# Kernel optimization log

Measured on AMD Instinct MI355X. Metric: run time of the kernel, lower is better.

The kernel has to match this reference:

```python
import jax, jax.numpy as jnp
import numpy as np

HORIZON = 60
HID = 128

def setup_inputs() -> dict:
    key = jax.random.key(0)
    ks = jax.random.split(key, 7)
    B, D, O = 16384, 256, 3
    s_ih = 1.0 / np.sqrt(HID)
    return {
        "x": jax.random.normal(ks[0], (B, D), jnp.float32),
        "W_ih": jax.random.normal(ks[1], (3 * HID, D), jnp.float32) * s_ih,
        "W_hh": jax.random.normal(ks[2], (3 * HID, HID), jnp.float32) * s_ih,
        "b_ih": jax.random.normal(ks[3], (3 * HID,), jnp.float32) * s_ih,
        "b_hh": jax.random.normal(ks[4], (3 * HID,), jnp.float32) * s_ih,
        "W_out": jax.random.normal(ks[5], (O, HID), jnp.float32) * s_ih,
        "b_out": jax.random.normal(ks[6], (O,), jnp.float32) * s_ih,
    }

def reference(x, W_ih, W_hh, b_ih, b_hh, W_out, b_out):
    # Input is identical at every timestep -> precompute input projection once.
    B = x.shape[0]
    gi = x @ W_ih.T + b_ih                      # [B, 3H]
    gi_r, gi_z, gi_n = jnp.split(gi, 3, axis=-1)

    def step(h, _):
        gh = h @ W_hh.T + b_hh                  # [B, 3H]
        gh_r, gh_z, gh_n = jnp.split(gh, 3, axis=-1)
        r = jax.nn.sigmoid(gi_r + gh_r)
        z = jax.nn.sigmoid(gi_z + gh_z)
        n = jnp.tanh(gi_n + r * gh_n)
        h_new = (1.0 - z) * n + z * h           # torch GRU update
        return h_new, h_new

    h0 = jnp.zeros((B, HID), x.dtype)
    _, hs = jax.lax.scan(step, h0, None, length=HORIZON)   # [T, B, H]
    out = jnp.einsum('tbh,oh->bto', hs, W_out) + b_out     # [B, T, O]
    return out
```

## Files before the change

### kernel.cpp

```cpp
#include <hip/hip_runtime.h>


typedef __attribute__((ext_vector_type(8))) short short8;
typedef __attribute__((ext_vector_type(4))) float f32x4;

#define MFMA16(a, b, c) __builtin_amdgcn_mfma_f32_16x16x32_bf16((a), (b), (c), 0, 0, 0)

__device__ __forceinline__ short f2bf(float x) {
    union { float f; unsigned u; } v; v.f = x;
    unsigned r = v.u + 0x7FFFu + ((v.u >> 16) & 1u);
    return (short)(r >> 16);
}
__device__ __forceinline__ unsigned pk2bf(float lo, float hi) {
    return ((unsigned)(unsigned short)f2bf(hi) << 16) | (unsigned short)f2bf(lo);
}

__device__ __forceinline__ short8 cvt8(const float* __restrict__ p) {
    f32x4 a = *(const f32x4*)p;
    f32x4 b = *(const f32x4*)(p + 4);
    short8 r;
    r[0] = f2bf(a[0]); r[1] = f2bf(a[1]); r[2] = f2bf(a[2]); r[3] = f2bf(a[3]);
    r[4] = f2bf(b[0]); r[5] = f2bf(b[1]); r[6] = f2bf(b[2]); r[7] = f2bf(b[3]);
    return r;
}

__device__ __forceinline__ float fsig(float x) {
    float e = __builtin_amdgcn_exp2f(x * -1.442695041f);
    return __builtin_amdgcn_rcpf(1.0f + e);
}
__device__ __forceinline__ float ftanh_(float x) {
    float e = __builtin_amdgcn_exp2f(x * -2.885390082f);
    return 2.0f * __builtin_amdgcn_rcpf(1.0f + e) - 1.0f;
}

__global__ __launch_bounds__(512, 2) void gru_traj_kernel(
    const float* __restrict__ x,
    const float* __restrict__ W_ih,
    const float* __restrict__ W_hh,
    const float* __restrict__ b_ih,
    const float* __restrict__ b_hh,
    const float* __restrict__ W_out,
    const float* __restrict__ b_out,
    float* __restrict__ out)
{
    const int tid  = threadIdx.x;
    const int wid  = tid >> 6;
    const int lane = tid & 63;
    const int l15  = lane & 15;
    const int l4   = lane >> 4;
    const int b0   = blockIdx.x << 6;
    const int hb   = wid << 4;

    __shared__ short hbuf[2][64 * 128];
    __shared__ short wobuf[3 * 136];

    {
        int* z = (int*)hbuf[0];
        #pragma unroll
        for (int i = 0; i < 8; ++i) z[tid + i * 512] = 0;
    }
    if (tid < 384) wobuf[(tid >> 7) * 136 + (tid & 127)] = f2bf(W_out[tid]);

    short8 wfrag[3][4];
    #pragma unroll
    for (int g = 0; g < 3; ++g)
        #pragma unroll
        for (int kt = 0; kt < 4; ++kt)
            wfrag[g][kt] = cvt8(W_hh + (size_t)(g * 128 + hb + l15) * 128 + kt * 32 + l4 * 8);

    const f32x4 bR4  = *(const f32x4*)(b_ih +       hb + l4 * 4) + *(const f32x4*)(b_hh +       hb + l4 * 4);
    const f32x4 bZ4  = *(const f32x4*)(b_ih + 128 + hb + l4 * 4) + *(const f32x4*)(b_hh + 128 + hb + l4 * 4);
    const f32x4 bN4i = *(const f32x4*)(b_ih + 256 + hb + l4 * 4);
    const f32x4 bN4h = *(const f32x4*)(b_hh + 256 + hb + l4 * 4);
    const float bo0 = b_out[0], bo1 = b_out[1], bo2 = b_out[2];

    f32x4 initR[4], initZ[4], giN[4];
    #pragma unroll
    for (int q = 0; q < 4; ++q) { initR[q] = bR4; initZ[q] = bZ4; giN[q] = bN4i; }
    #pragma unroll
    for (int kt = 0; kt < 8; ++kt) {
        short8 a0 = cvt8(W_ih + (size_t)(      hb + l15) * 256 + kt * 32 + l4 * 8);
        short8 a1 = cvt8(W_ih + (size_t)(128 + hb + l15) * 256 + kt * 32 + l4 * 8);
        short8 a2 = cvt8(W_ih + (size_t)(256 + hb + l15) * 256 + kt * 32 + l4 * 8);
        #pragma unroll
        for (int q = 0; q < 4; ++q) {
            short8 bx = cvt8(x + (size_t)(b0 + q * 16 + l15) * 256 + kt * 32 + l4 * 8);
            initR[q] = MFMA16(a0, bx, initR[q]);
            initZ[q] = MFMA16(a1, bx, initZ[q]);
            giN [q] = MFMA16(a2, bx, giN [q]);
        }
    }

    float hq[4][4];
    #pragma unroll
    for (int q = 0; q < 4; ++q)
        #pragma unroll
        for (int r = 0; r < 4; ++r) hq[q][r] = 0.f;

    const int s8  = (wid << 2) | l4;
    const int wsw = (((s8 >> 1) ^ l15) & 15);

    __syncthreads();

    #pragma unroll 2
    for (int t = 0; t < 60; ++t) {
        const short* rb = hbuf[t & 1];
        short*       wb = hbuf[(t & 1) ^ 1];
        #pragma unroll
        for (int q = 0; q < 4; ++q) {
            short8 af[4];
            #pragma unroll
            for (int kt = 0; kt < 4; ++kt)
                af[kt] = *(const short8*)(rb + (q * 16 + l15) * 128 + (((kt * 4 + l4) ^ l15) & 15) * 8);

            if (t > 0 && wid == ((q + t) & 7)) {
                f32x4 oa = (f32x4){0.f, 0.f, 0.f, 0.f};
                #pragma unroll
                for (int kt = 0; kt < 4; ++kt) {
                    short8 wo = {0, 0, 0, 0, 0, 0, 0, 0};
                    if (l15 < 3) wo = *(const short8*)(wobuf + l15 * 136 + kt * 32 + l4 * 8);
                    oa = MFMA16(wo, af[kt], oa);
                }
                if (l4 == 0) {
                    float* op = out + (size_t)(b0 + q * 16 + l15) * 180 + (t - 1) * 3;
                    op[0] = oa[0] + bo0; op[1] = oa[1] + bo1; op[2] = oa[2] + bo2;
                }
            }

            f32x4 aR = initR[q], aZ = initZ[q], aN = bN4h;
            #pragma unroll
            for (int kt = 0; kt < 4; ++kt) {
                aR = MFMA16(wfrag[0][kt], af[kt], aR);
                aZ = MFMA16(wfrag[1][kt], af[kt], aZ);
                aN = MFMA16(wfrag[2][kt], af[kt], aN);
            }
            float hn[4];
            #pragma unroll
            for (int r = 0; r < 4; ++r) {
                float rr = fsig(aR[r]);
                float zz = fsig(aZ[r]);
                float nn = ftanh_(giN[q][r] + rr * aN[r]);
                hn[r] = nn + zz * (hq[q][r] - nn);
                hq[q][r] = hn[r];
            }
            uint2 pk;
            pk.x = pk2bf(hn[0], hn[1]);
            pk.y = pk2bf(hn[2], hn[3]);
            *(uint2*)(wb + (q * 16 + l15) * 128 + wsw * 8 + (s8 & 1) * 4) = pk;
        }
        __syncthreads();
    }

    if (wid < 4) {
        const int q = wid;
        const short* rb = hbuf[0];
        f32x4 oa = (f32x4){0.f, 0.f, 0.f, 0.f};
        #pragma unroll
        for (int kt = 0; kt < 4; ++kt) {
            short8 af = *(const short8*)(rb + (q * 16 + l15) * 128 + (((kt * 4 + l4) ^ l15) & 15) * 8);
            short8 wo = {0, 0, 0, 0, 0, 0, 0, 0};
            if (l15 < 3) wo = *(const short8*)(wobuf + l15 * 136 + kt * 32 + l4 * 8);
            oa = MFMA16(wo, af, oa);
        }
        if (l4 == 0) {
            float* op = out + (size_t)(b0 + q * 16 + l15) * 180 + 59 * 3;
            op[0] = oa[0] + bo0; op[1] = oa[1] + bo1; op[2] = oa[2] + bo2;
        }
    }
}

extern "C" void kernel_launch(void* const* d_in, const int* in_sizes, int n_in,
                              void* d_out, int out_size, void* d_ws, size_t ws_size,
                              hipStream_t stream) {
    const float* x     = (const float*)d_in[0];
    const float* W_ih  = (const float*)d_in[1];
    const float* W_hh  = (const float*)d_in[2];
    const float* b_ih  = (const float*)d_in[3];
    const float* b_hh  = (const float*)d_in[4];
    const float* W_out = (const float*)d_in[5];
    const float* b_out = (const float*)d_in[6];
    float* out = (float*)d_out;

    const int B = in_sizes[0] / 256;
    hipLaunchKernelGGL(gru_traj_kernel, dim3(B / 64), dim3(512), 0, stream,
                       x, W_ih, W_hh, b_ih, b_hh, W_out, b_out, out);
}
```

Measured before the change: 167.6 us.

## Shrink GRU blocks to 32 rows, 4 waves each owning 32 hidden units

Each block now handles 32 batch rows with 4 waves instead of 64 rows with 8 waves. Each wave computes two 16-unit hidden tiles, so every A-fragment of h read from LDS feeds twice as many MFMAs and the per-step barrier covers fewer waves. The gate math now shares one reciprocal between the r and z sigmoids, and packing uses the hardware v_cvt_pk_bf16_f32 instruction. In exchange each wave holds twice as many weight fragments in registers, and the grid grows to twice as many smaller blocks.

```diff
diff --git a/kernel.cpp b/kernel.cpp
--- a/kernel.cpp
+++ b/kernel.cpp
@@ -11,8 +11,11 @@
     unsigned r = v.u + 0x7FFFu + ((v.u >> 16) & 1u);
     return (short)(r >> 16);
 }
-__device__ __forceinline__ unsigned pk2bf(float lo, float hi) {
-    return ((unsigned)(unsigned short)f2bf(hi) << 16) | (unsigned short)f2bf(lo);
+
+__device__ __forceinline__ unsigned cvtpk(float lo, float hi) {
+    unsigned d;
+    asm("v_cvt_pk_bf16_f32 %0, %1, %2" : "=v"(d) : "v"(lo), "v"(hi));
+    return d;
 }
 
 __device__ __forceinline__ short8 cvt8(const float* __restrict__ p) {
@@ -24,16 +27,7 @@
     return r;
 }
 
-__device__ __forceinline__ float fsig(float x) {
-    float e = __builtin_amdgcn_exp2f(x * -1.442695041f);
-    return __builtin_amdgcn_rcpf(1.0f + e);
-}
-__device__ __forceinline__ float ftanh_(float x) {
-    float e = __builtin_amdgcn_exp2f(x * -2.885390082f);
-    return 2.0f * __builtin_amdgcn_rcpf(1.0f + e) - 1.0f;
-}
-
-__global__ __launch_bounds__(512, 2) void gru_traj_kernel(
+__global__ __launch_bounds__(256, 2) void gru_traj_kernel(
     const float* __restrict__ x,
     const float* __restrict__ W_ih,
     const float* __restrict__ W_hh,
@@ -48,57 +42,75 @@
     const int lane = tid & 63;
     const int l15  = lane & 15;
     const int l4   = lane >> 4;
-    const int b0   = blockIdx.x << 6;
-    const int hb   = wid << 4;
-
-    __shared__ short hbuf[2][64 * 128];
+    const int b0   = blockIdx.x << 5;
+    const int hb   = wid << 5;
+
+    __shared__ short hbuf[2][32 * 128];
     __shared__ short wobuf[3 * 136];
 
     {
         int* z = (int*)hbuf[0];
         #pragma unroll
-        for (int i = 0; i < 8; ++i) z[tid + i * 512] = 0;
-    }
-    if (tid < 384) wobuf[(tid >> 7) * 136 + (tid & 127)] = f2bf(W_out[tid]);
-
-    short8 wfrag[3][4];
-    #pragma unroll
-    for (int g = 0; g < 3; ++g)
-        #pragma unroll
-        for (int kt = 0; kt < 4; ++kt)
-            wfrag[g][kt] = cvt8(W_hh + (size_t)(g * 128 + hb + l15) * 128 + kt * 32 + l4 * 8);
-
-    const f32x4 bR4  = *(const f32x4*)(b_ih +       hb + l4 * 4) + *(const f32x4*)(b_hh +       hb + l4 * 4);
-    const f32x4 bZ4  = *(const f32x4*)(b_ih + 128 + hb + l4 * 4) + *(const f32x4*)(b_hh + 128 + hb + l4 * 4);
-    const f32x4 bN4i = *(const f32x4*)(b_ih + 256 + hb + l4 * 4);
-    const f32x4 bN4h = *(const f32x4*)(b_hh + 256 + hb + l4 * 4);
+        for (int i = 0; i < 8; ++i) z[tid + i * 256] = 0;
+    }
+    for (int i = tid; i < 384; i += 256)
+        wobuf[(i >> 7) * 136 + (i & 127)] = f2bf(W_out[i]);
+
+    short8 wfrag[2][3][4];
+    #pragma unroll
+    for (int m = 0; m < 2; ++m)
+        #pragma unroll
+        for (int g = 0; g < 3; ++g)
+            #pragma unroll
+            for (int kt = 0; kt < 4; ++kt)
+                wfrag[m][g][kt] = cvt8(W_hh + (size_t)(g * 128 + hb + m * 16 + l15) * 128 + kt * 32 + l4 * 8);
+
+    f32x4 bNh[2];
+    f32x4 bR[2], bZ[2], bNi[2];
+    #pragma unroll
+    for (int m = 0; m < 2; ++m) {
+        const int base = hb + m * 16 + l4 * 4;
+        bR[m]  = *(const f32x4*)(b_ih + base)       + *(const f32x4*)(b_hh + base);
+        bZ[m]  = *(const f32x4*)(b_ih + 128 + base) + *(const f32x4*)(b_hh + 128 + base);
+        bNi[m] = *(const f32x4*)(b_ih + 256 + base);
+        bNh[m] = *(const f32x4*)(b_hh + 256 + base);
+    }
     const float bo0 = b_out[0], bo1 = b_out[1], bo2 = b_out[2];
 
-    f32x4 initR[4], initZ[4], giN[4];
-    #pragma unroll
-    for (int q = 0; q < 4; ++q) { initR[q] = bR4; initZ[q] = bZ4; giN[q] = bN4i; }
+    f32x4 initR[2][2], initZ[2][2], giN[2][2];
+    #pragma unroll
+    for (int q = 0; q < 2; ++q)
+        #pragma unroll
+        for (int m = 0; m < 2; ++m) { initR[q][m] = bR[m]; initZ[q][m] = bZ[m]; giN[q][m] = bNi[m]; }
     #pragma unroll
     for (int kt = 0; kt < 8; ++kt) {
-        short8 a0 = cvt8(W_ih + (size_t)(      hb + l15) * 256 + kt * 32 + l4 * 8);
-        short8 a1 = cvt8(W_ih + (size_t)(128 + hb + l15) * 256 + kt * 32 + l4 * 8);
-        short8 a2 = cvt8(W_ih + (size_t)(256 + hb + l15) * 256 + kt * 32 + l4 * 8);
-        #pragma unroll
-        for (int q = 0; q < 4; ++q) {
+        short8 a_[2][3];
+        #pragma unroll
+        for (int m = 0; m < 2; ++m)
+            #pragma unroll
+            for (int g = 0; g < 3; ++g)
+                a_[m][g] = cvt8(W_ih + (size_t)(g * 128 + hb + m * 16 + l15) * 256 + kt * 32 + l4 * 8);
+        #pragma unroll
+        for (int q = 0; q < 2; ++q) {
             short8 bx = cvt8(x + (size_t)(b0 + q * 16 + l15) * 256 + kt * 32 + l4 * 8);
-            initR[q] = MFMA16(a0, bx, initR[q]);
-            initZ[q] = MFMA16(a1, bx, initZ[q]);
-            giN [q] = MFMA16(a2, bx, giN [q]);
-        }
-    }
-
-    float hq[4][4];
-    #pragma unroll
-    for (int q = 0; q < 4; ++q)
-        #pragma unroll
-        for (int r = 0; r < 4; ++r) hq[q][r] = 0.f;
-
-    const int s8  = (wid << 2) | l4;
-    const int wsw = (((s8 >> 1) ^ l15) & 15);
+            #pragma unroll
+            for (int m = 0; m < 2; ++m) {
+                initR[q][m] = MFMA16(a_[m][0], bx, initR[q][m]);
+                initZ[q][m] = MFMA16(a_[m][1], bx, initZ[q][m]);
+                giN [q][m] = MFMA16(a_[m][2], bx, giN [q][m]);
+            }
+        }
+    }
+
+    float hq[2][2][4];
+    #pragma unroll
+    for (int q = 0; q < 2; ++q)
+        #pragma unroll
+        for (int m = 0; m < 2; ++m)
+            #pragma unroll
+            for (int r = 0; r < 4; ++r) hq[q][m][r] = 0.f;
+
+    const float nL2E = -1.442695041f;
 
     __syncthreads();
 
@@ -107,13 +119,13 @@
         const short* rb = hbuf[t & 1];
         short*       wb = hbuf[(t & 1) ^ 1];
         #pragma unroll
-        for (int q = 0; q < 4; ++q) {
+        for (int q = 0; q < 2; ++q) {
             short8 af[4];
             #pragma unroll
             for (int kt = 0; kt < 4; ++kt)
                 af[kt] = *(const short8*)(rb + (q * 16 + l15) * 128 + (((kt * 4 + l4) ^ l15) & 15) * 8);
 
-            if (t > 0 && wid == ((q + t) & 7)) {
+            if (t > 0 && wid == ((q + t) & 3)) {
                 f32x4 oa = (f32x4){0.f, 0.f, 0.f, 0.f};
                 #pragma unroll
                 for (int kt = 0; kt < 4; ++kt) {
@@ -127,31 +139,41 @@
                 }
             }
 
-            f32x4 aR = initR[q], aZ = initZ[q], aN = bN4h;
-            #pragma unroll
-            for (int kt = 0; kt < 4; ++kt) {
-                aR = MFMA16(wfrag[0][kt], af[kt], aR);
-                aZ = MFMA16(wfrag[1][kt], af[kt], aZ);
-                aN = MFMA16(wfrag[2][kt], af[kt], aN);
+            #pragma unroll
+            for (int m = 0; m < 2; ++m) {
+                f32x4 aR = initR[q][m], aZ = initZ[q][m], aN = bNh[m];
+                #pragma unroll
+                for (int kt = 0; kt < 4; ++kt) {
+                    aR = MFMA16(wfrag[m][0][kt], af[kt], aR);
+                    aZ = MFMA16(wfrag[m][1][kt], af[kt], aZ);
+                    aN = MFMA16(wfrag[m][2][kt], af[kt], aN);
+                }
+                float hn[4];
+                #pragma unroll
+                for (int r = 0; r < 4; ++r) {
+                    float eA = __builtin_amdgcn_exp2f(aR[r] * nL2E);
+                    float eB = __builtin_amdgcn_exp2f(aZ[r] * nL2E);
+                    float A  = 1.0f + eA, Bv = 1.0f + eB;
+                    float R  = __builtin_amdgcn_rcpf(A * Bv);
+                    float rr = R * Bv;
+                    float zz = R * A;
+                    float sn = fmaf(rr, aN[r], giN[q][m][r]);
+                    float eC = __builtin_amdgcn_exp2f(sn * (2.0f * nL2E));
+                    float nn = fmaf(2.0f, __builtin_amdgcn_rcpf(1.0f + eC), -1.0f);
+                    hn[r] = fmaf(zz, hq[q][m][r] - nn, nn);
+                    hq[q][m][r] = hn[r];
+                }
+                uint2 pk;
+                pk.x = cvtpk(hn[0], hn[1]);
+                pk.y = cvtpk(hn[2], hn[3]);
+                const int s8 = (wid << 3) | (m << 2) | l4;
+                *(uint2*)(wb + (q * 16 + l15) * 128 + (((s8 >> 1) ^ l15) & 15) * 8 + (s8 & 1) * 4) = pk;
             }
-            float hn[4];
-            #pragma unroll
-            for (int r = 0; r < 4; ++r) {
-                float rr = fsig(aR[r]);
-                float zz = fsig(aZ[r]);
-                float nn = ftanh_(giN[q][r] + rr * aN[r]);
-                hn[r] = nn + zz * (hq[q][r] - nn);
-                hq[q][r] = hn[r];
-            }
-            uint2 pk;
-            pk.x = pk2bf(hn[0], hn[1]);
-            pk.y = pk2bf(hn[2], hn[3]);
-            *(uint2*)(wb + (q * 16 + l15) * 128 + wsw * 8 + (s8 & 1) * 4) = pk;
         }
         __syncthreads();
     }
 
-    if (wid < 4) {
+    if (wid < 2) {
         const int q = wid;
         const short* rb = hbuf[0];
         f32x4 oa = (f32x4){0.f, 0.f, 0.f, 0.f};
@@ -182,6 +204,6 @@
     float* out = (float*)d_out;
 
     const int B = in_sizes[0] / 256;
-    hipLaunchKernelGGL(gru_traj_kernel, dim3(B / 64), dim3(512), 0, stream,
+    hipLaunchKernelGGL(gru_traj_kernel, dim3(B / 32), dim3(256), 0, stream,
                        x, W_ih, W_hh, b_ih, b_hh, W_out, b_out, out);
 }
```

Result: slower. 174.2 us (+3.9%).

## Halve batch per block, raise occupancy, fold sigmoid scaling into weights

Applied to the files above, without the earlier changes.

Each block now handles 32 batch rows instead of 64, doubling the grid and raising launch bounds to 4 blocks per CU. The R/Z input projections move from registers to shared memory to cut register pressure. The sigmoid prescale is folded into W_hh, W_ih and the biases, two sigmoids share one reciprocal, and bf16 packing uses a hardware convert instruction. The risks are extra LDS reads every step, tighter register budgets, and slightly different rounding.

```diff
diff --git a/kernel.cpp b/kernel.cpp
--- a/kernel.cpp
+++ b/kernel.cpp
@@ -11,8 +11,11 @@
     unsigned r = v.u + 0x7FFFu + ((v.u >> 16) & 1u);
     return (short)(r >> 16);
 }
-__device__ __forceinline__ unsigned pk2bf(float lo, float hi) {
-    return ((unsigned)(unsigned short)f2bf(hi) << 16) | (unsigned short)f2bf(lo);
+
+__device__ __forceinline__ unsigned cvtpk(float lo, float hi) {
+    unsigned d;
+    asm("v_cvt_pk_bf16_f32 %0, %1, %2" : "=v"(d) : "v"(lo), "v"(hi));
+    return d;
 }
 
 __device__ __forceinline__ short8 cvt8(const float* __restrict__ p) {
@@ -23,17 +26,16 @@
     r[4] = f2bf(b[0]); r[5] = f2bf(b[1]); r[6] = f2bf(b[2]); r[7] = f2bf(b[3]);
     return r;
 }
-
-__device__ __forceinline__ float fsig(float x) {
-    float e = __builtin_amdgcn_exp2f(x * -1.442695041f);
-    return __builtin_amdgcn_rcpf(1.0f + e);
-}
-__device__ __forceinline__ float ftanh_(float x) {
-    float e = __builtin_amdgcn_exp2f(x * -2.885390082f);
-    return 2.0f * __builtin_amdgcn_rcpf(1.0f + e) - 1.0f;
-}
-
-__global__ __launch_bounds__(512, 2) void gru_traj_kernel(
+__device__ __forceinline__ short8 cvt8s(const float* __restrict__ p, float s) {
+    f32x4 a = *(const f32x4*)p;
+    f32x4 b = *(const f32x4*)(p + 4);
+    short8 r;
+    r[0] = f2bf(a[0] * s); r[1] = f2bf(a[1] * s); r[2] = f2bf(a[2] * s); r[3] = f2bf(a[3] * s);
+    r[4] = f2bf(b[0] * s); r[5] = f2bf(b[1] * s); r[6] = f2bf(b[2] * s); r[7] = f2bf(b[3] * s);
+    return r;
+}
+
+__global__ __launch_bounds__(512, 4) void gru_traj_kernel(
     const float* __restrict__ x,
     const float* __restrict__ W_ih,
     const float* __restrict__ W_hh,
@@ -48,57 +50,70 @@
     const int lane = tid & 63;
     const int l15  = lane & 15;
     const int l4   = lane >> 4;
-    const int b0   = blockIdx.x << 6;
+    const int b0   = blockIdx.x << 5;
     const int hb   = wid << 4;
 
-    __shared__ short hbuf[2][64 * 128];
+    const float SCL  = -1.442695041f;
+    const float SCL2 = -2.885390082f;
+
+    __shared__ short hbuf[2][32 * 128];
+    __shared__ float gibuf[2 * 8 * 2 * 256];
     __shared__ short wobuf[3 * 136];
 
     {
         int* z = (int*)hbuf[0];
         #pragma unroll
-        for (int i = 0; i < 8; ++i) z[tid + i * 512] = 0;
+        for (int i = 0; i < 4; ++i) z[tid + i * 512] = 0;
     }
     if (tid < 384) wobuf[(tid >> 7) * 136 + (tid & 127)] = f2bf(W_out[tid]);
 
     short8 wfrag[3][4];
     #pragma unroll
-    for (int g = 0; g < 3; ++g)
-        #pragma unroll
-        for (int kt = 0; kt < 4; ++kt)
-            wfrag[g][kt] = cvt8(W_hh + (size_t)(g * 128 + hb + l15) * 128 + kt * 32 + l4 * 8);
-
-    const f32x4 bR4  = *(const f32x4*)(b_ih +       hb + l4 * 4) + *(const f32x4*)(b_hh +       hb + l4 * 4);
-    const f32x4 bZ4  = *(const f32x4*)(b_ih + 128 + hb + l4 * 4) + *(const f32x4*)(b_hh + 128 + hb + l4 * 4);
-    const f32x4 bN4i = *(const f32x4*)(b_ih + 256 + hb + l4 * 4);
-    const f32x4 bN4h = *(const f32x4*)(b_hh + 256 + hb + l4 * 4);
+    for (int kt = 0; kt < 4; ++kt) {
+        wfrag[0][kt] = cvt8s(W_hh + (size_t)(      hb + l15) * 128 + kt * 32 + l4 * 8, SCL);
+        wfrag[1][kt] = cvt8s(W_hh + (size_t)(128 + hb + l15) * 128 + kt * 32 + l4 * 8, SCL);
+        wfrag[2][kt] = cvt8 (W_hh + (size_t)(256 + hb + l15) * 128 + kt * 32 + l4 * 8);
+    }
+
+    const int bbase = hb + l4 * 4;
+    const f32x4 bR4 = (*(const f32x4*)(b_ih + bbase)       + *(const f32x4*)(b_hh + bbase))       * SCL;
+    const f32x4 bZ4 = (*(const f32x4*)(b_ih + 128 + bbase) + *(const f32x4*)(b_hh + 128 + bbase)) * SCL;
+    const f32x4 bNi = *(const f32x4*)(b_ih + 256 + bbase);
+    const f32x4 bNh = *(const f32x4*)(b_hh + 256 + bbase);
     const float bo0 = b_out[0], bo1 = b_out[1], bo2 = b_out[2];
 
-    f32x4 initR[4], initZ[4], giN[4];
+    f32x4 giN[2];
+    {
+        f32x4 initR[2], initZ[2];
+        #pragma unroll
+        for (int q = 0; q < 2; ++q) { initR[q] = bR4; initZ[q] = bZ4; giN[q] = bNi; }
+        #pragma unroll
+        for (int kt = 0; kt < 8; ++kt) {
+            short8 a0 = cvt8s(W_ih + (size_t)(      hb + l15) * 256 + kt * 32 + l4 * 8, SCL);
+            short8 a1 = cvt8s(W_ih + (size_t)(128 + hb + l15) * 256 + kt * 32 + l4 * 8, SCL);
+            short8 a2 = cvt8 (W_ih + (size_t)(256 + hb + l15) * 256 + kt * 32 + l4 * 8);
+            #pragma unroll
+            for (int q = 0; q < 2; ++q) {
+                short8 bx = cvt8(x + (size_t)(b0 + q * 16 + l15) * 256 + kt * 32 + l4 * 8);
+                initR[q] = MFMA16(a0, bx, initR[q]);
+                initZ[q] = MFMA16(a1, bx, initZ[q]);
+                giN [q] = MFMA16(a2, bx, giN [q]);
+            }
+        }
+        #pragma unroll
+        for (int q = 0; q < 2; ++q) {
+            *(f32x4*)(gibuf + ((0 * 8 + wid) * 2 + q) * 256 + lane * 4) = initR[q];
+            *(f32x4*)(gibuf + ((1 * 8 + wid) * 2 + q) * 256 + lane * 4) = initZ[q];
+        }
+    }
+
+    float hq[2][4];
     #pragma unroll
-    for (int q = 0; q < 4; ++q) { initR[q] = bR4; initZ[q] = bZ4; giN[q] = bN4i; }
-    #pragma unroll
-    for (int kt = 0; kt < 8; ++kt) {
-        short8 a0 = cvt8(W_ih + (size_t)(      hb + l15) * 256 + kt * 32 + l4 * 8);
-        short8 a1 = cvt8(W_ih + (size_t)(128 + hb + l15) * 256 + kt * 32 + l4 * 8);
-        short8 a2 = cvt8(W_ih + (size_t)(256 + hb + l15) * 256 + kt * 32 + l4 * 8);
-        #pragma unroll
-        for (int q = 0; q < 4; ++q) {
-            short8 bx = cvt8(x + (size_t)(b0 + q * 16 + l15) * 256 + kt * 32 + l4 * 8);
-            initR[q] = MFMA16(a0, bx, initR[q]);
-            initZ[q] = MFMA16(a1, bx, initZ[q]);
-            giN [q] = MFMA16(a2, bx, giN [q]);
-        }
-    }
-
-    float hq[4][4];
-    #pragma unroll
-    for (int q = 0; q < 4; ++q)
+    for (int q = 0; q < 2; ++q)
         #pragma unroll
         for (int r = 0; r < 4; ++r) hq[q][r] = 0.f;
 
-    const int s8  = (wid << 2) | l4;
-    const int wsw = (((s8 >> 1) ^ l15) & 15);
+    const int s8 = (wid << 2) | l4;
 
     __syncthreads();
 
@@ -107,7 +122,7 @@
         const short* rb = hbuf[t & 1];
         short*       wb = hbuf[(t & 1) ^ 1];
         #pragma unroll
-        for (int q = 0; q < 4; ++q) {
+        for (int q = 0; q < 2; ++q) {
             short8 af[4];
             #pragma unroll
             for (int kt = 0; kt < 4; ++kt)
@@ -127,7 +142,9 @@
                 }
             }
 
-            f32x4 aR = initR[q], aZ = initZ[q], aN = bN4h;
+            f32x4 aR = *(const f32x4*)(gibuf + ((0 * 8 + wid) * 2 + q) * 256 + lane * 4);
+            f32x4 aZ = *(const f32x4*)(gibuf + ((1 * 8 + wid) * 2 + q) * 256 + lane * 4);
+            f32x4 aN = bNh;
             #pragma unroll
             for (int kt = 0; kt < 4; ++kt) {
                 aR = MFMA16(wfrag[0][kt], af[kt], aR);
@@ -137,21 +154,27 @@
             float hn[4];
             #pragma unroll
             for (int r = 0; r < 4; ++r) {
-                float rr = fsig(aR[r]);
-                float zz = fsig(aZ[r]);
-                float nn = ftanh_(giN[q][r] + rr * aN[r]);
-                hn[r] = nn + zz * (hq[q][r] - nn);
+                float eA = __builtin_amdgcn_exp2f(aR[r]);
+                float eB = __builtin_amdgcn_exp2f(aZ[r]);
+                float A  = 1.0f + eA, Bv = 1.0f + eB;
+                float R  = __builtin_amdgcn_rcpf(A * Bv);
+                float rr = R * Bv;
+                float zz = R * A;
+                float sn = fmaf(rr, aN[r], giN[q][r]);
+                float eC = __builtin_amdgcn_exp2f(sn * SCL2);
+                float nn = fmaf(2.0f, __builtin_amdgcn_rcpf(1.0f + eC), -1.0f);
+                hn[r] = fmaf(zz, hq[q][r] - nn, nn);
                 hq[q][r] = hn[r];
             }
             uint2 pk;
-            pk.x = pk2bf(hn[0], hn[1]);
-            pk.y = pk2bf(hn[2], hn[3]);
-            *(uint2*)(wb + (q * 16 + l15) * 128 + wsw * 8 + (s8 & 1) * 4) = pk;
+            pk.x = cvtpk(hn[0], hn[1]);
+            pk.y = cvtpk(hn[2], hn[3]);
+            *(uint2*)(wb + (q * 16 + l15) * 128 + (((s8 >> 1) ^ l15) & 15) * 8 + (s8 & 1) * 4) = pk;
         }
         __syncthreads();
     }
 
-    if (wid < 4) {
+    if (wid < 2) {
         const int q = wid;
         const short* rb = hbuf[0];
         f32x4 oa = (f32x4){0.f, 0.f, 0.f, 0.f};
@@ -182,6 +205,6 @@
     float* out = (float*)d_out;
 
     const int B = in_sizes[0] / 256;
-    hipLaunchKernelGGL(gru_traj_kernel, dim3(B / 64), dim3(512), 0, stream,
+    hipLaunchKernelGGL(gru_traj_kernel, dim3(B / 32), dim3(512), 0, stream,
                        x, W_ih, W_hh, b_ih, b_hh, W_out, b_out, out);
 }
```

Result: no change. 167.3 us (-0.2%).
